# Performance work log

Measured on AMD Instinct MI355X. Metric: run time of the kernel, lower is better.

Reference implementation:

```python
import jax, jax.numpy as jnp
import numpy as np

NUM_CLASSES = 80
NUM_TOP_QUERIES = 300
MASK_THRESHOLD = 0.5
OUT_SIZE = 480  # fixed original image size (all orig_target_sizes == 480)


def setup_inputs() -> dict:
    key = jax.random.key(0)
    k1, k2, k3 = jax.random.split(key, 3)
    B, Q, C, Hm, Wm = 2, 300, NUM_CLASSES, 128, 128
    pred_logits = jax.random.normal(k1, (B, Q, C), dtype=jnp.float32)
    pred_boxes = jax.random.uniform(k2, (B, Q, 4), dtype=jnp.float32)  # cxcywh in [0,1]
    pred_masks = jax.random.normal(k3, (B, Q, Hm, Wm), dtype=jnp.float32)
    orig_target_sizes = jnp.ones((B, 2), dtype=jnp.float32) * OUT_SIZE
    return {
        'pred_logits': pred_logits,
        'pred_boxes': pred_boxes,
        'pred_masks': pred_masks,
        'orig_target_sizes': orig_target_sizes,
    }


def _box_cxcywh_to_xyxy(boxes):
    cx, cy, w, h = jnp.split(boxes, 4, axis=-1)
    return jnp.concatenate([cx - 0.5 * w, cy - 0.5 * h, cx + 0.5 * w, cy + 0.5 * h], axis=-1)


def reference(pred_logits, pred_boxes, pred_masks, orig_target_sizes):
    B, Q, C = pred_logits.shape
    Hm, Wm = pred_masks.shape[-2:]
    K = NUM_TOP_QUERIES

    # box conversion + scaling to original image size ([s0,s1,s0,s1] like repeat(1,2))
    scale = jnp.tile(orig_target_sizes, (1, 2))[:, None, :]  # [B,1,4]
    scaled_boxes = _box_cxcywh_to_xyxy(pred_boxes) * scale    # [B,Q,4]

    # focal-loss path: sigmoid scores, flattened top-k over (Q*C)
    scores = jax.nn.sigmoid(pred_logits).reshape(B, Q * C)
    top_scores, top_indices = jax.lax.top_k(scores, K)        # [B,K]
    top_labels = top_indices % C
    query_indices = top_indices // C                          # [B,K]

    selected_boxes = jnp.take_along_axis(scaled_boxes, query_indices[..., None], axis=1)  # [B,K,4]

    # per-sample mask selection + sigmoid + bilinear upsample (align_corners=False)
    sel_masks = jnp.take_along_axis(pred_masks, query_indices[..., None, None], axis=1)   # [B,K,Hm,Wm]
    mask_probs = jax.nn.sigmoid(sel_masks)
    up = jax.vmap(lambda m: jax.image.resize(m, (OUT_SIZE, OUT_SIZE), 'bilinear'))(
        mask_probs.reshape(B * K, Hm, Wm)
    ).reshape(B, K, OUT_SIZE, OUT_SIZE)
    binary_masks = up > MASK_THRESHOLD                        # [B,K,H,W] bool (torch adds channel dim of 1)

    return top_scores, top_labels, selected_boxes, binary_masks
```

## Files before the change

kernel.cpp:

```cpp
#include <hip/hip_runtime.h>
#include <math.h>

#define BATCH 2
#define NQ    300
#define NC    80
#define NFLAT (NQ * NC)
#define TOPK  300
#define HM    128
#define OUTS  480
#define NBKT  4096
#define CAP   4096

#define HBLK  8
#define HTHR  512
#define CHUNK (NFLAT / HBLK)

#define INVSCALEF 0.26666668f

typedef float v4f __attribute__((ext_vector_type(4)));

__device__ __forceinline__ unsigned mapf(float x) {
    unsigned u = __float_as_uint(x);
    return (u & 0x80000000u) ? ~u : (u | 0x80000000u);
}

__global__ __launch_bounds__(HTHR) void hist_kernel(
    const float* __restrict__ logits,
    unsigned* __restrict__ ghist)
{
    __shared__ unsigned h[NBKT];
    const int blk = blockIdx.x;
    const int b = blk / HBLK, sub = blk % HBLK;
    const float* lg = logits + (size_t)b * NFLAT + (size_t)sub * CHUNK;

    for (int i = threadIdx.x; i < NBKT; i += HTHR) h[i] = 0;
    __syncthreads();
    for (int i = threadIdx.x; i < CHUNK; i += HTHR)
        atomicAdd(&h[mapf(lg[i]) >> 20], 1u);
    __syncthreads();
    unsigned* dst = ghist + (size_t)blk * NBKT;
    for (int i = threadIdx.x; i < NBKT; i += HTHR) dst[i] = h[i];
}

__global__ __launch_bounds__(1024) void select_kernel(
    const float* __restrict__ logits,
    const float* __restrict__ boxes,
    const float* __restrict__ osize,
    const unsigned* __restrict__ ghist,
    float* __restrict__ out,
    int* __restrict__ qidx)
{
    __shared__ unsigned hist[NBKT];
    __shared__ unsigned long long cand[CAP];
    __shared__ unsigned psum[1024];
    __shared__ unsigned sh_T;
    __shared__ unsigned sh_cnt;

    const int b = blockIdx.x;
    const int tid = threadIdx.x;
    const float* lg = logits + (size_t)b * NFLAT;

    for (int i = tid; i < NBKT; i += 1024) {
        unsigned s = 0;
        #pragma unroll
        for (int k = 0; k < HBLK; ++k)
            s += ghist[(size_t)(b * HBLK + k) * NBKT + i];
        hist[i] = s;
    }
    if (tid == 0) sh_cnt = 0;
    __syncthreads();

    psum[tid] = hist[4 * tid] + hist[4 * tid + 1] + hist[4 * tid + 2] + hist[4 * tid + 3];
    __syncthreads();
    for (unsigned off = 1; off < 1024; off <<= 1) {
        unsigned v = (tid + off < 1024) ? psum[tid + off] : 0u;
        __syncthreads();
        psum[tid] += v;
        __syncthreads();
    }
    {
        unsigned nxt = (tid == 1023) ? 0u : psum[tid + 1];
        if (psum[tid] >= (unsigned)TOPK && nxt < (unsigned)TOPK) {
            unsigned acc = nxt, T = 4u * (unsigned)tid;
            for (int bk = 4 * tid + 3; bk >= 4 * tid; --bk) {
                if (acc + hist[bk] >= (unsigned)TOPK) { T = (unsigned)bk; break; }
                acc += hist[bk];
            }
            sh_T = T;
        }
    }
    __syncthreads();
    const unsigned T = sh_T;

    for (int i = tid; i < NFLAT; i += 1024) {
        unsigned m = mapf(lg[i]);
        if ((m >> 20) >= T) {
            unsigned pos = atomicAdd(&sh_cnt, 1u);
            if (pos < CAP)
                cand[pos] = ((unsigned long long)m << 32)
                          | (unsigned long long)(0xFFFFFFFFu - (unsigned)i);
        }
    }
    __syncthreads();
    const unsigned cnt = (sh_cnt > CAP) ? CAP : sh_cnt;

    for (unsigned t = tid; t < cnt; t += 1024) {
        const unsigned long long my = cand[t];
        unsigned rank = 0;
        for (unsigned j = 0; j < cnt; ++j) rank += (cand[j] > my) ? 1u : 0u;
        if (rank < (unsigned)TOPK) {
            unsigned idx = 0xFFFFFFFFu - (unsigned)(my & 0xFFFFFFFFull);
            int q = (int)(idx / NC);
            int c = (int)(idx % NC);
            double x = (double)lg[idx];
            double score = 1.0 / (1.0 + exp(-x));

            out[b * TOPK + rank] = (float)score;
            out[BATCH * TOPK + b * TOPK + rank] = (float)c;

            const float* bx = boxes + ((size_t)(b * NQ + q)) * 4;
            double cx = (double)bx[0], cy = (double)bx[1];
            double w  = (double)bx[2], h  = (double)bx[3];
            double s0 = (double)osize[b * 2 + 0];
            double s1 = (double)osize[b * 2 + 1];
            float* ob = out + 2 * BATCH * TOPK + ((size_t)(b * TOPK + rank)) * 4;
            ob[0] = (float)((cx - 0.5 * w) * s0);
            ob[1] = (float)((cy - 0.5 * h) * s1);
            ob[2] = (float)((cx + 0.5 * w) * s0);
            ob[3] = (float)((cy + 0.5 * h) * s1);

            qidx[b * TOPK + rank] = q;
        }
    }
}

#define VROWS   16
#define NVS     (OUTS / VROWS)
#define MAXR    6

__global__ __launch_bounds__(256) void mask_kernel(
    const float* __restrict__ masks,
    const int* __restrict__ qidx,
    float* __restrict__ outm)
{
    __shared__ float sig[MAXR * HM];

    const int tid = threadIdx.x;
    const int unit = blockIdx.x;
    const int mask_id = unit / NVS;
    const int vs = unit % NVS;
    const int ys = vs * VROWS;
    const int b = mask_id / TOPK;
    const int q = qidx[mask_id];

    float s_first = ((float)ys + 0.5f) * INVSCALEF - 0.5f;
    float s_last  = ((float)(ys + VROWS - 1) + 0.5f) * INVSCALEF - 0.5f;
    int r_lo = (int)floorf(s_first);
    if (r_lo < 0) r_lo = 0; if (r_lo > HM - 2) r_lo = HM - 2;
    int r_hi = (int)floorf(s_last);
    if (r_hi < 0) r_hi = 0; if (r_hi > HM - 2) r_hi = HM - 2;
    r_hi += 1;
    const int cnt = r_hi - r_lo + 1;

    const v4f* s4 = (const v4f*)(masks
                      + ((size_t)(b * NQ + q)) * (HM * HM)
                      + (size_t)r_lo * HM);
    const int n4 = cnt * (HM / 4);
    if (tid < n4) {
        v4f v = s4[tid];
        float* dst = sig + tid * 4;
        dst[0] = 1.0f / (1.0f + __expf(-v.x));
        dst[1] = 1.0f / (1.0f + __expf(-v.y));
        dst[2] = 1.0f / (1.0f + __expf(-v.z));
        dst[3] = 1.0f / (1.0f + __expf(-v.w));
    }

    const int qd = tid % 120;
    const int yy = tid / 120;
    const int x0 = qd * 4;
    int c0 = 0, ar[4];
    float fxr[4];
    #pragma unroll
    for (int j = 0; j < 4; ++j) {
        float sx = ((float)(x0 + j) + 0.5f) * INVSCALEF - 0.5f;
        int jx = (int)floorf(sx);
        if (jx < 0) jx = 0; if (jx > HM - 2) jx = HM - 2;
        float f = sx - (float)jx;
        f = fminf(fmaxf(f, 0.0f), 1.0f);
        if (j == 0) c0 = jx;
        ar[j]  = jx - c0;
        fxr[j] = f;
    }
    const int c1 = c0 + 1;
    const int c2 = (c0 + 2 > HM - 1) ? (HM - 1) : (c0 + 2);

    __syncthreads();

    if (tid < 240) {
        float* outp = outm + (size_t)mask_id * (OUTS * OUTS)
                           + (size_t)(ys + yy) * OUTS + x0;
        #pragma unroll
        for (int it = 0; it < VROWS / 2; ++it) {
            const int y = ys + yy + it * 2;
            float sy = ((float)y + 0.5f) * INVSCALEF - 0.5f;
            int jy = (int)floorf(sy);
            if (jy < 0) jy = 0; if (jy > HM - 2) jy = HM - 2;
            float fy = sy - (float)jy;
            fy = fminf(fmaxf(fy, 0.0f), 1.0f);

            const float* r0 = sig + (size_t)(jy - r_lo) * HM;
            const float* r1 = r0 + HM;
            const float wy1 = fy, wy0 = 1.0f - fy;

            const float t0 = wy0 * r0[c0] + wy1 * r1[c0];
            const float t1 = wy0 * r0[c1] + wy1 * r1[c1];
            const float t2 = wy0 * r0[c2] + wy1 * r1[c2];

            v4f res;
            #pragma unroll
            for (int j = 0; j < 4; ++j) {
                const float ta = ar[j] ? t1 : t0;
                const float tb = ar[j] ? t2 : t1;
                const float val = ta + fxr[j] * (tb - ta);
                res[j] = (val > 0.5f) ? 1.0f : 0.0f;
            }
            *((v4f*)(outp + (size_t)(it * 2) * OUTS)) = res;
        }
    }
}

extern "C" void kernel_launch(void* const* d_in, const int* in_sizes, int n_in,
                              void* d_out, int out_size, void* d_ws, size_t ws_size,
                              hipStream_t stream) {
    const float* logits = (const float*)d_in[0];
    const float* boxes  = (const float*)d_in[1];
    const float* masks  = (const float*)d_in[2];
    const float* osize  = (const float*)d_in[3];
    float* out = (float*)d_out;

    int* qidx = (int*)d_ws;
    unsigned* ghist = (unsigned*)((char*)d_ws + 4096);

    hist_kernel<<<BATCH * HBLK, HTHR, 0, stream>>>(logits, ghist);
    select_kernel<<<BATCH, 1024, 0, stream>>>(logits, boxes, osize, ghist, out, qidx);

    mask_kernel<<<BATCH * TOPK * NVS, 256, 0, stream>>>(masks, qidx, out + 3600);
}
```

Before: 149.1 us.

## Replace tiled shared-memory mask upsample with grid-stride per-quad kernel

The mask kernel no longer stages sigmoid rows in shared memory per 16-row tile. It becomes a fixed-size grid-stride loop where each thread handles one 4-pixel output quad. Each thread loads the six needed source values directly from global memory, recomputes the sigmoids and interpolates, which removes block syncs and the many small blocks. In exchange it does redundant global loads and exp work, relying on the cache to absorb the reuse.

```diff
diff --git a/kernel.cpp b/kernel.cpp
--- a/kernel.cpp
+++ b/kernel.cpp
@@ -134,98 +134,65 @@
     }
 }
 
-#define VROWS   16
-#define NVS     (OUTS / VROWS)
-#define MAXR    6
-
-__global__ __launch_bounds__(256) void mask_kernel(
+#define QPM   (120 * OUTS)
+#define TOTQ  (BATCH * TOPK * QPM)
+#define MGRID 2048
+#define MTHR  256
+
+__global__ __launch_bounds__(MTHR) void mask_kernel(
     const float* __restrict__ masks,
     const int* __restrict__ qidx,
     float* __restrict__ outm)
 {
-    __shared__ float sig[MAXR * HM];
-
-    const int tid = threadIdx.x;
-    const int unit = blockIdx.x;
-    const int mask_id = unit / NVS;
-    const int vs = unit % NVS;
-    const int ys = vs * VROWS;
-    const int b = mask_id / TOPK;
-    const int q = qidx[mask_id];
-
-    float s_first = ((float)ys + 0.5f) * INVSCALEF - 0.5f;
-    float s_last  = ((float)(ys + VROWS - 1) + 0.5f) * INVSCALEF - 0.5f;
-    int r_lo = (int)floorf(s_first);
-    if (r_lo < 0) r_lo = 0; if (r_lo > HM - 2) r_lo = HM - 2;
-    int r_hi = (int)floorf(s_last);
-    if (r_hi < 0) r_hi = 0; if (r_hi > HM - 2) r_hi = HM - 2;
-    r_hi += 1;
-    const int cnt = r_hi - r_lo + 1;
-
-    const v4f* s4 = (const v4f*)(masks
-                      + ((size_t)(b * NQ + q)) * (HM * HM)
-                      + (size_t)r_lo * HM);
-    const int n4 = cnt * (HM / 4);
-    if (tid < n4) {
-        v4f v = s4[tid];
-        float* dst = sig + tid * 4;
-        dst[0] = 1.0f / (1.0f + __expf(-v.x));
-        dst[1] = 1.0f / (1.0f + __expf(-v.y));
-        dst[2] = 1.0f / (1.0f + __expf(-v.z));
-        dst[3] = 1.0f / (1.0f + __expf(-v.w));
-    }
-
-    const int qd = tid % 120;
-    const int yy = tid / 120;
-    const int x0 = qd * 4;
-    int c0 = 0, ar[4];
-    float fxr[4];
-    #pragma unroll
-    for (int j = 0; j < 4; ++j) {
-        float sx = ((float)(x0 + j) + 0.5f) * INVSCALEF - 0.5f;
-        int jx = (int)floorf(sx);
-        if (jx < 0) jx = 0; if (jx > HM - 2) jx = HM - 2;
-        float f = sx - (float)jx;
-        f = fminf(fmaxf(f, 0.0f), 1.0f);
-        if (j == 0) c0 = jx;
-        ar[j]  = jx - c0;
-        fxr[j] = f;
-    }
-    const int c1 = c0 + 1;
-    const int c2 = (c0 + 2 > HM - 1) ? (HM - 1) : (c0 + 2);
-
-    __syncthreads();
-
-    if (tid < 240) {
-        float* outp = outm + (size_t)mask_id * (OUTS * OUTS)
-                           + (size_t)(ys + yy) * OUTS + x0;
+    const unsigned stride = MGRID * MTHR;
+    for (unsigned i = blockIdx.x * MTHR + threadIdx.x; i < TOTQ; i += stride) {
+        const unsigned mask_id = i / QPM;
+        const unsigned rem = i - mask_id * QPM;
+        const unsigned y  = rem / 120;
+        const unsigned qd = rem - y * 120;
+        const int x0 = (int)qd * 4;
+        const int b = (mask_id >= TOPK) ? 1 : 0;
+        const int q = qidx[mask_id];
+        const float* __restrict__ src = masks + ((size_t)(b * NQ + q)) * (HM * HM);
+
+        float sy = ((float)y + 0.5f) * INVSCALEF - 0.5f;
+        int jy = (int)floorf(sy);
+        if (jy < 0) jy = 0; if (jy > HM - 2) jy = HM - 2;
+        float fy = fminf(fmaxf(sy - (float)jy, 0.0f), 1.0f);
+
+        float sx0 = ((float)x0 + 0.5f) * INVSCALEF - 0.5f;
+        int c0 = (int)floorf(sx0);
+        if (c0 < 0) c0 = 0; if (c0 > HM - 2) c0 = HM - 2;
+        const int c2 = (c0 + 2 > HM - 1) ? (HM - 1) : (c0 + 2);
+
+        const float* r0 = src + (size_t)jy * HM;
+        const float* r1 = r0 + HM;
+        const float a00 = r0[c0], a01 = r0[c0 + 1], a02 = r0[c2];
+        const float a10 = r1[c0], a11 = r1[c0 + 1], a12 = r1[c2];
+
+        const float s00 = 1.0f / (1.0f + __expf(-a00));
+        const float s01 = 1.0f / (1.0f + __expf(-a01));
+        const float s02 = 1.0f / (1.0f + __expf(-a02));
+        const float s10 = 1.0f / (1.0f + __expf(-a10));
+        const float s11 = 1.0f / (1.0f + __expf(-a11));
+        const float s12 = 1.0f / (1.0f + __expf(-a12));
+        const float t0 = s00 + fy * (s10 - s00);
+        const float t1 = s01 + fy * (s11 - s01);
+        const float t2 = s02 + fy * (s12 - s02);
+
+        v4f res;
         #pragma unroll
-        for (int it = 0; it < VROWS / 2; ++it) {
-            const int y = ys + yy + it * 2;
-            float sy = ((float)y + 0.5f) * INVSCALEF - 0.5f;
-            int jy = (int)floorf(sy);
-            if (jy < 0) jy = 0; if (jy > HM - 2) jy = HM - 2;
-            float fy = sy - (float)jy;
-            fy = fminf(fmaxf(fy, 0.0f), 1.0f);
-
-            const float* r0 = sig + (size_t)(jy - r_lo) * HM;
-            const float* r1 = r0 + HM;
-            const float wy1 = fy, wy0 = 1.0f - fy;
-
-            const float t0 = wy0 * r0[c0] + wy1 * r1[c0];
-            const float t1 = wy0 * r0[c1] + wy1 * r1[c1];
-            const float t2 = wy0 * r0[c2] + wy1 * r1[c2];
-
-            v4f res;
-            #pragma unroll
-            for (int j = 0; j < 4; ++j) {
-                const float ta = ar[j] ? t1 : t0;
-                const float tb = ar[j] ? t2 : t1;
-                const float val = ta + fxr[j] * (tb - ta);
-                res[j] = (val > 0.5f) ? 1.0f : 0.0f;
-            }
-            *((v4f*)(outp + (size_t)(it * 2) * OUTS)) = res;
-        }
+        for (int j = 0; j < 4; ++j) {
+            float sx = ((float)(x0 + j) + 0.5f) * INVSCALEF - 0.5f;
+            int jx = (int)floorf(sx);
+            if (jx < 0) jx = 0; if (jx > HM - 2) jx = HM - 2;
+            float fx = fminf(fmaxf(sx - (float)jx, 0.0f), 1.0f);
+            const float ta = (jx > c0) ? t1 : t0;
+            const float tb = (jx > c0) ? t2 : t1;
+            const float val = ta + fx * (tb - ta);
+            res[j] = (val > 0.5f) ? 1.0f : 0.0f;
+        }
+        *((v4f*)(outm + (size_t)i * 4)) = res;
     }
 }
 
@@ -244,5 +211,5 @@
     hist_kernel<<<BATCH * HBLK, HTHR, 0, stream>>>(logits, ghist);
     select_kernel<<<BATCH, 1024, 0, stream>>>(logits, boxes, osize, ghist, out, qidx);
 
-    mask_kernel<<<BATCH * TOPK * NVS, 256, 0, stream>>>(masks, qidx, out + 3600);
-}
+    mask_kernel<<<MGRID, MTHR, 0, stream>>>(masks, qidx, out + 3600);
+}
```

After: 254.5 us. 70.7% more time.
